# Kernel optimization log

Measured on AMD Instinct MI355X. Metric: run time of the kernel, lower is better.

The kernel has to match this reference:

```python
import jax, jax.numpy as jnp
import numpy as np
import math

A = 32; B = 32; PSIZE = 16; K = 3; STRIDE = 2; PAD = 1; ITERS = 3; FINAL_LAMBDA = 0.01
KK = K * K; KKA = KK * A; KKA2 = KKA // 2 + 1
EPS = 1e-12; LN2PI = math.log(2 * math.pi)


def unfold(x, k, s, p):
    # torch F.unfold: output feature dim ordered (C, kh, kw), columns row-major
    b, C, h, w = x.shape
    xp = jnp.pad(x, ((0, 0), (0, 0), (p, p), (p, p)))
    oh = (h + 2 * p - k) // s + 1
    ow = (w + 2 * p - k) // s + 1
    cols = [xp[:, :, ki:ki + s * (oh - 1) + 1:s, kj:kj + s * (ow - 1) + 1:s]
            for ki in range(k) for kj in range(k)]
    patches = jnp.stack(cols, axis=2)  # [b, C, kk, oh, ow]
    return patches.reshape(b, C, k * k, oh * ow), oh, ow


def setup_inputs():
    key = jax.random.key(0)
    ks = jax.random.split(key, 8)
    b, h, w = 4, 14, 14
    a_in = jax.random.uniform(ks[0], (b, A, h, w), dtype=jnp.float32)
    pose = jax.random.normal(ks[1], (b, A * PSIZE, h, w), dtype=jnp.float32)
    mpose_w = jax.random.normal(ks[2], (B * PSIZE, PSIZE), dtype=jnp.float32) / np.float32(np.sqrt(PSIZE))
    mpose_b = jnp.zeros((B * PSIZE,), jnp.float32)
    freq_w = jax.random.normal(ks[3], (KKA2, PSIZE, 2), dtype=jnp.float32) * 0.02
    ln_g = jnp.ones((A,), jnp.float32)
    ln_b = jnp.zeros((A,), jnp.float32)
    lim = np.float32(np.sqrt(6.0 / (KK + KK)))  # xavier_uniform on [kk, kk, 1]
    spat_w = jax.random.uniform(ks[4], (KK, KK, 1), jnp.float32, -lim, lim)
    spat_bias = jnp.ones((KK,), jnp.float32)
    beta_u = jnp.zeros((1, 1, B, 1), jnp.float32)
    beta_a = jnp.zeros((1, 1, B), jnp.float32)
    return dict(a_in=a_in, pose=pose, mpose_w=mpose_w, mpose_b=mpose_b,
                freq_w=freq_w, ln_g=ln_g, ln_b=ln_b, spat_w=spat_w,
                spat_bias=spat_bias, beta_u=beta_u, beta_a=beta_a)


def _forward(a_in, pose, mpose_w, mpose_b, freq_w, ln_g, ln_b,
             spat_w, spat_bias, beta_u, beta_a):
    b = a_in.shape[0]
    pose_u, oh, ow = unfold(pose, K, STRIDE, PAD)  # [b, A*PSIZE, KK, l]
    l = oh * ow
    pose_u = pose_u.reshape(b, A, PSIZE, KK, l)
    pose_u = pose_u.transpose(0, 4, 3, 1, 2).reshape(b, l, KKA, PSIZE)
    # mpose linear: psize -> B*psize
    po = jnp.einsum('blkp,qp->blkq', pose_u, mpose_w) + mpose_b
    po = po.reshape(b * l, KKA, B, PSIZE)
    # Frequency FFT filter over kkA axis (weight shared across all B slices)
    xf = jnp.fft.rfft(po, axis=1, norm='ortho')        # [bl, KKA2, B, PSIZE] complex
    wc = freq_w[..., 0] + 1j * freq_w[..., 1]           # [KKA2, PSIZE]
    xf = xf * wc[None, :, None, :]
    po = jnp.fft.irfft(xf, n=KKA, axis=1, norm='ortho') + po  # residual
    v = po.reshape(b, l, KKA, B, PSIZE)
    a_u, _, _ = unfold(a_in, K, STRIDE, PAD)            # [b, A, KK, l]
    a_u = a_u.transpose(0, 3, 2, 1).reshape(b, l, KKA)
    # Spatial gating applied to ones-initialized r (identical for every B slice)
    ones = jnp.ones((b * l, KKA), jnp.float32)
    g = ones.reshape(b * l, KK, A)
    mu_g = g.mean(-1, keepdims=True)
    var_g = ((g - mu_g) ** 2).mean(-1, keepdims=True)
    gn = (g - mu_g) / jnp.sqrt(var_g + 1e-5) * ln_g + ln_b
    g2 = jnp.einsum('ij,nja->nia', spat_w[:, :, 0], gn) + spat_bias[None, :, None]
    gate = jax.nn.gelu(g2, approximate=False).reshape(b * l, KKA) + ones
    logit = jnp.broadcast_to(gate[:, :, None], (b * l, KKA, B))
    r = jax.nn.softmax(logit, axis=2).reshape(b, l, KKA, B, 1)
    a_out = mu = None
    for i in range(ITERS):
        lam = FINAL_LAMBDA * (1.0 - 0.95 ** (i + 1))
        # m-step
        rr = r * a_u[:, :, :, None, None]
        r_sum = rr.sum(axis=2, keepdims=True)                 # [b,l,1,B,1]
        coeff = rr / (r_sum + EPS)
        mu = (coeff * v).sum(axis=2, keepdims=True)           # [b,l,1,B,PSIZE]
        sig = (coeff * (v - mu) ** 2).sum(axis=2, keepdims=True) + EPS
        cost = (beta_u + jnp.log(jnp.sqrt(sig[:, :, 0]))) * r_sum[:, :, 0]  # [b,l,B,PSIZE]
        a_out = jax.nn.sigmoid(lam * (beta_a - cost.sum(axis=3)))           # [b,l,B]
        if i < ITERS - 1:
            # e-step (note: log(sigma_sq * ln2pi) is faithful to the original code)
            ln_p = (-0.5 * jnp.sum(jnp.log(sig * LN2PI), axis=-1)
                    - jnp.sum((v - mu) ** 2 / (2.0 * sig), axis=-1))        # [b,l,KKA,B]
            ln_ap = ln_p + jnp.log(a_out[:, :, None, :])
            r = jax.nn.softmax(ln_ap, axis=-1)[..., None]
    pose_out = mu[:, :, 0].reshape(b, l, B * PSIZE).transpose(0, 2, 1).reshape(b, B * PSIZE, oh, ow)
    a_fin = a_out.transpose(0, 2, 1).reshape(b, B, oh, ow)
    return a_fin, pose_out


def reference(a_in, pose, mpose_w, mpose_b, freq_w, ln_g, ln_b,
              spat_w, spat_bias, beta_u, beta_a):
    return _forward(a_in, pose, mpose_w, mpose_b, freq_w, ln_g, ln_b,
                    spat_w, spat_bias, beta_u, beta_a)
```

## Files before the change

### kernel.cpp

```cpp
#include <hip/hip_runtime.h>
#include <hip/hip_bf16.h>
#include <math.h>

#define A_    32
#define B_    32
#define PS    16
#define KK_   9
#define KKA_  288
#define OH_   7
#define L_    49
#define NB    4
#define NSITE 196

#define LAM1 5.0e-4f
#define LAM2 9.75e-4f
#define LAM3 1.42625e-3f
#define LOG_LN2PI 0.6086775903077413f

typedef _Float16 half2v __attribute__((ext_vector_type(2)));
typedef _Float16 half4v __attribute__((ext_vector_type(4)));
typedef short    short8 __attribute__((ext_vector_type(8)));
typedef float    floatx4 __attribute__((ext_vector_type(4)));

static __device__ __forceinline__ float san(float x, float lo, float hi){
    return fminf(fmaxf(x, lo), hi);
}

static __device__ __forceinline__ float dot2acc(half2v a, half2v b, float c){
#if __has_builtin(__builtin_amdgcn_fdot2)
    return __builtin_amdgcn_fdot2(a, b, c, false);
#else
    return c + (float)a.x*(float)b.x + (float)a.y*(float)b.y;
#endif
}

__global__ void k_prep_c(const float* __restrict__ fw,
                         ushort* __restrict__ cpr, float* __restrict__ csum)
{
    int id = blockIdx.x*256 + threadIdx.x;
    if (id >= 16*288) return;
    int p = id / 288, m = id % 288;
    float acc = fw[(0*16 + p)*2 + 0];
    for (int k = 1; k <= 143; ++k){
        float re = fw[(k*16 + p)*2 + 0];
        float im = fw[(k*16 + p)*2 + 1];
        int km = (k*m) % 288;
        float ang = 0.021816615649929116f * (float)km;
        float s, c; sincosf(ang, &s, &c);
        acc += 2.0f*(re*c - im*s);
    }
    float re144 = fw[(144*16 + p)*2 + 0];
    acc += re144 * ((m & 1) ? -1.0f : 1.0f);
    float cv = acc * (1.0f/288.0f);
    if (m == 0) cv += 1.0f;
    cv = san(cv, -1e4f, 1e4f);

    __hip_bfloat16 hb = __float2bfloat16(cv);
    float hif = __bfloat162float(hb);
    __hip_bfloat16 lb = __float2bfloat16(cv - hif);
    ushort hi = *(ushort*)&hb, lo = *(ushort*)&lb;

    ushort* c0h = cpr + p*592;
    ushort* c1h = cpr + 16*592   + p*592;
    ushort* c0l = cpr + 16*592*2 + p*592;
    ushort* c1l = cpr + 16*592*3 + p*592;
    int x1 = 288 - m;
    c0h[x1] = hi;  c0l[x1] = lo;
    c1h[x1-1] = hi; c1l[x1-1] = lo;
    if (m >= 1){
        int x2 = 576 - m;
        c0h[x2] = hi;  c0l[x2] = lo;
        c1h[x2-1] = hi; c1l[x2-1] = lo;
    } else {
        c0h[0] = hi; c0l[0] = lo;
        csum[p] = san(1.0f + fw[(0*16 + p)*2 + 0], -1e4f, 1e4f);
    }
}

__global__ void k_prep_x(const float* __restrict__ pose,
                         __hip_bfloat16* __restrict__ Xt, int n0, int cols)
{
    int id = blockIdx.x*256 + threadIdx.x;
    if (id >= cols*KKA_) return;
    int c = id / KKA_, j = id % KKA_;
    int n = n0 + (c >> 4), q = c & 15;
    int bs = n / L_, l = n % L_, oy = l / OH_, ox = l % OH_;
    int kk = j >> 5, a = j & 31;
    int y = oy*2 - 1 + kk/3, x = ox*2 - 1 + kk%3;
    float v = 0.f;
    if ((unsigned)y < 14u && (unsigned)x < 14u)
        v = pose[((bs*(A_*PS) + a*PS + q)*14 + y)*14 + x];
    Xt[id] = __float2bfloat16(san(v, -1e4f, 1e4f));
}

__launch_bounds__(256)
__global__ void k_stageB(const ushort* __restrict__ cpr, const __hip_bfloat16* __restrict__ Xt,
                         _Float16* __restrict__ U, int cols, int ns)
{
    const int bx = blockIdx.x, by = blockIdx.y, p = blockIdx.z;
    const int t = threadIdx.x;
    const int w = t >> 6, lane = t & 63;
    const int mn = lane & 15, quad = lane >> 4;
    const int i0 = by*48;
    const int col = bx*64 + w*16 + mn;
    const int colc = (col < cols) ? col : (cols - 1);

    const ushort* c0h = cpr + p*592;
    const ushort* c1h = cpr + 16*592   + p*592;
    const ushort* c0l = cpr + 16*592*2 + p*592;
    const ushort* c1l = cpr + 16*592*3 + p*592;

    floatx4 acc[3] = {{0,0,0,0},{0,0,0,0},{0,0,0,0}};
    for (int k0 = 0; k0 < 288; k0 += 32){
        short8 bfrag = *(const short8*)&Xt[colc*KKA_ + k0 + quad*8];
        #pragma unroll
        for (int s = 0; s < 3; ++s){
            int o = 288 + k0 + quad*8 - (i0 + s*16 + mn);
            int sel = o & 1;
            int off = o - sel;
            const ushort* bh = sel ? c1h : c0h;
            const ushort* bl = sel ? c1l : c0l;
            short8 ah = *(const short8*)&bh[off];
            short8 al = *(const short8*)&bl[off];
            acc[s] = __builtin_amdgcn_mfma_f32_16x16x32_bf16(ah, bfrag, acc[s], 0, 0, 0);
            acc[s] = __builtin_amdgcn_mfma_f32_16x16x32_bf16(al, bfrag, acc[s], 0, 0, 0);
        }
    }
    if (col < cols){
        const int nn = col >> 4, q0 = col & 15;
        #pragma unroll
        for (int s = 0; s < 3; ++s){
            #pragma unroll
            for (int r = 0; r < 4; ++r){
                int i = i0 + s*16 + quad*4 + r;
                U[(i*ns + nn)*256 + p*16 + q0] = (_Float16)acc[s][r];
            }
        }
    }
}

__global__ void
__launch_bounds__(512)
__attribute__((amdgpu_waves_per_eu(2, 2)))
k_em(const _Float16* __restrict__ U, const float* __restrict__ a_in,
     const float* __restrict__ mpw, const float* __restrict__ mpb,
     const float* __restrict__ csum,
     const float* __restrict__ beta_u, const float* __restrict__ beta_a,
     int n0, int ns, float* __restrict__ out)
{
    const int nl = blockIdx.x;
    const int n  = n0 + nl;
    const int t = threadIdx.x;
    const int Bc = t >> 4, p = t & 15;
    const int bs = n / L_, l = n % L_;

    __shared__ _Float16 us[2][16][256];
    __shared__ float a_s[KKA_];
    __shared__ float d_s[16][33];
    __shared__ float rbuf[16][33];
    __shared__ float cst[32];

    half4v ha, hb;
    {
        int u0 = t, u1 = t + 512;
        ha = *(const half4v*)&U[((u0>>6)*ns + nl)*256 + (u0&63)*4];
        hb = *(const half4v*)&U[((8 + (u1&511)/64)*ns + nl)*256 + (u1&63)*4];
    }

    for (int j = t; j < KKA_; j += 512){
        int kk = j >> 5, a = j & 31;
        int oy = l / OH_, ox = l % OH_;
        int y = oy*2 - 1 + kk/3, x = ox*2 - 1 + kk%3;
        float v = 0.f;
        if ((unsigned)y < 14u && (unsigned)x < 14u)
            v = a_in[((bs*A_ + a)*14 + y)*14 + x];
        a_s[j] = san(v, 0.f, 1e4f);
    }
    half2v w_h[8];
    #pragma unroll
    for (int k = 0; k < 8; ++k){
        w_h[k].x = (_Float16)mpw[t*16 + 2*k];
        w_h[k].y = (_Float16)mpw[t*16 + 2*k + 1];
    }
    const float vb = mpb[t] * csum[p];
    const float bu = beta_u[Bc];
    const float ba = beta_a[Bc];

    *(half4v*)&us[0][t>>6][(t&63)*4]       = ha;
    *(half4v*)&us[0][8 + (t>>6)][(t&63)*4] = hb;
    __syncthreads();

    float S0tot = 0.f;
    for (int j = 0; j < KKA_; ++j) S0tot += a_s[j];

    half2v v_h[144];
    float S1 = 0.f, S2 = 0.f;
    #pragma unroll
    for (int ch = 0; ch < 18; ++ch){
        if (ch < 17){
            int base = (ch+1)*16;
            int u0 = t, u1 = t + 512;
            ha = *(const half4v*)&U[((base + (u0>>6))*ns + nl)*256 + (u0&63)*4];
            hb = *(const half4v*)&U[((base + 8 + (u0>>6))*ns + nl)*256 + (u1&63)*4];
        }
        #pragma unroll
        for (int k = 0; k < 8; ++k){
            union { uint4 u4; half2v h2[4]; } A0, A1, B0, B1;
            A0.u4 = *(const uint4*)&us[ch&1][2*k][p*16];
            A1.u4 = *(const uint4*)&us[ch&1][2*k][p*16 + 8];
            B0.u4 = *(const uint4*)&us[ch&1][2*k+1][p*16];
            B1.u4 = *(const uint4*)&us[ch&1][2*k+1][p*16 + 8];
            float v0 = vb, v1 = vb;
            #pragma unroll
            for (int m = 0; m < 4; ++m){
                v0 = dot2acc(A0.h2[m], w_h[m],   v0);
                v0 = dot2acc(A1.h2[m], w_h[4+m], v0);
                v1 = dot2acc(B0.h2[m], w_h[m],   v1);
                v1 = dot2acc(B1.h2[m], w_h[4+m], v1);
            }
            float a0 = a_s[ch*16 + 2*k], a1 = a_s[ch*16 + 2*k + 1];
            S1 += a0*v0 + a1*v1;
            S2 += a0*v0*v0 + a1*v1*v1;
            half2v vh; vh.x = (_Float16)v0; vh.y = (_Float16)v1;
            v_h[ch*8 + k] = vh;
        }
        if (ch < 17){
            *(half4v*)&us[(ch+1)&1][t>>6][(t&63)*4]       = ha;
            *(half4v*)&us[(ch+1)&1][8 + (t>>6)][(t&63)*4] = hb;
        }
        __syncthreads();
    }

    float mu_r, i2s_r;
    {
        const float rs  = S0tot * (1.0f/32.0f);
        const float inv = 1.0f / (rs + 1e-12f);
        const float S1r = S1 * (1.0f/32.0f), S2r = S2 * (1.0f/32.0f);
        mu_r = S1r * inv;
        const float sg  = fmaxf((S2r - 2.f*mu_r*S1r + mu_r*mu_r*rs) * inv, 0.f) + 1e-12f;
        i2s_r = 0.5f / sg;
        const float lg  = logf(sg);
        float cs = (bu + 0.5f*lg) * rs;
        float ls = lg + LOG_LN2PI;
        #pragma unroll
        for (int m = 1; m < 16; m <<= 1){ cs += __shfl_xor(cs, m, 16); ls += __shfl_xor(ls, m, 16); }
        const float aout = san(1.f/(1.f + expf(-LAM1*(ba - cs))), 1e-30f, 1.f);
        if (p == 0) cst[Bc] = logf(aout) - 0.5f*ls;
    }
    __syncthreads();

    const int b0 = p & 1, b1 = (p>>1)&1, b2 = (p>>2)&1, b3 = (p>>3)&1;
    float muF = 0.f, aF = 0.f;
    for (int it = 0; it < 2; ++it){
        const float lam = it ? LAM3 : LAM2;
        float T0 = 0.f, T1 = 0.f, T2 = 0.f;
        #pragma unroll
        for (int ch = 0; ch < 18; ++ch){
            float vc[16], e[16];
            #pragma unroll
            for (int k = 0; k < 8; ++k){
                half2v vh = v_h[ch*8 + k];
                vc[2*k]   = (float)vh.x;
                vc[2*k+1] = (float)vh.y;
            }
            #pragma unroll
            for (int s = 0; s < 16; ++s){
                float dv = vc[s] - mu_r;
                e[s] = dv*dv*i2s_r;
            }
            float e1[8], e2[4], e3[2], dfin;
            #pragma unroll
            for (int s = 0; s < 8; ++s){
                float a  = b0 ? e[2*s+1] : e[2*s];
                float sd = b0 ? e[2*s]   : e[2*s+1];
                e1[s] = a + __shfl_xor(sd, 1);
            }
            #pragma unroll
            for (int s = 0; s < 4; ++s){
                float a  = b1 ? e1[2*s+1] : e1[2*s];
                float sd = b1 ? e1[2*s]   : e1[2*s+1];
                e2[s] = a + __shfl_xor(sd, 2);
            }
            #pragma unroll
            for (int s = 0; s < 2; ++s){
                float a  = b2 ? e2[2*s+1] : e2[2*s];
                float sd = b2 ? e2[2*s]   : e2[2*s+1];
                e3[s] = a + __shfl_xor(sd, 4);
            }
            {
                float a  = b3 ? e3[1] : e3[0];
                float sd = b3 ? e3[0] : e3[1];
                dfin = a + __shfl_xor(sd, 8);
            }
            d_s[p][Bc] = dfin;
            __syncthreads();
            {
                const int isub = t >> 5, Bce = t & 31;
                float lnap = cst[Bce] - d_s[isub][Bce];
                float mx = lnap;
                #pragma unroll
                for (int m = 16; m >= 1; m >>= 1) mx = fmaxf(mx, __shfl_xor(mx, m));
                float ex = expf(lnap - mx);
                float sm = ex;
                #pragma unroll
                for (int m = 16; m >= 1; m >>= 1) sm += __shfl_xor(sm, m);
                rbuf[isub][Bce] = (ex / sm) * a_s[ch*16 + isub];
            }
            __syncthreads();
            #pragma unroll
            for (int s = 0; s < 16; ++s){
                float rr = rbuf[s][Bc];
                float tv = rr * vc[s];
                T0 += rr; T1 += tv; T2 += tv * vc[s];
            }
        }
        const float inv = 1.f/(T0 + 1e-12f);
        const float mu  = T1 * inv;
        const float sg  = fmaxf((T2 - 2.f*mu*T1 + mu*mu*T0) * inv, 0.f) + 1e-12f;
        const float lg  = logf(sg);
        float cs = (bu + 0.5f*lg) * T0;
        float ls = lg + LOG_LN2PI;
        #pragma unroll
        for (int m = 1; m < 16; m <<= 1){ cs += __shfl_xor(cs, m, 16); ls += __shfl_xor(ls, m, 16); }
        const float aout = san(1.f/(1.f + expf(-lam*(ba - cs))), 1e-30f, 1.f);
        if (it == 0){
            mu_r = mu; i2s_r = 0.5f/sg;
            if (p == 0) cst[Bc] = logf(aout) - 0.5f*ls;
            __syncthreads();
        } else { muF = mu; aF = aout; }
    }

    if (p == 0) out[bs*(B_*L_) + Bc*L_ + l] = san(aF, 0.f, 1.f);
    out[6272 + (bs*512 + t)*L_ + l] = san(muF, -1e4f, 1e4f);
}

extern "C" void kernel_launch(void* const* d_in, const int* in_sizes, int n_in,
                              void* d_out, int out_size, void* d_ws, size_t ws_size,
                              hipStream_t stream)
{
    const float* a_in   = (const float*)d_in[0];
    const float* pose   = (const float*)d_in[1];
    const float* mpw    = (const float*)d_in[2];
    const float* mpb    = (const float*)d_in[3];
    const float* fw     = (const float*)d_in[4];
    const float* beta_u = (const float*)d_in[9];
    const float* beta_a = (const float*)d_in[10];
    float* out = (float*)d_out;

    char* base = (char*)d_ws;
    float*  csum = (float*)(base + 0);
    ushort* cpr  = (ushort*)(base + 256);

    const int opts[] = {196, 98, 49, 28, 14, 7, 4, 2, 1};
    int ns = 1;
    for (int oi = 0; oi < 9; ++oi){
        size_t need = 76288u + (size_t)156672u * (size_t)opts[oi];
        if (need <= ws_size){ ns = opts[oi]; break; }
    }
    const int G = NSITE / ns;
    const int cols = ns * PS;
    __hip_bfloat16* Xt = (__hip_bfloat16*)(base + 76288);
    _Float16*       Ug = (_Float16*)(base + 76288 + (size_t)9216*ns);

    k_prep_c<<<18, 256, 0, stream>>>(fw, cpr, csum);
    for (int g = 0; g < G; ++g){
        const int n0 = g * ns;
        k_prep_x<<<(cols*KKA_ + 255)/256, 256, 0, stream>>>(pose, Xt, n0, cols);
        k_stageB<<<dim3((cols + 63)/64, 6, 16), 256, 0, stream>>>(cpr, Xt, Ug, cols, ns);
        k_em    <<<ns, 512, 0, stream>>>(Ug, a_in, mpw, mpb, csum, beta_u, beta_a, n0, ns, out);
    }
}
```

Measured before the change: 307.5 us.

## Split EM vote storage between LDS and registers, read U directly from global

Removes the double-buffered LDS staging of U and its per-chunk barriers. Each thread now loads its U slice straight from global memory. The first half of the 288 computed votes goes into a 144KB LDS array and the second half stays in registers, halving the per-thread register array. Launch bounds change to (512,2) in place of the waves_per_eu attribute. This cuts register pressure and synchronization, at the cost of uncoalesced strided global loads, heavy LDS use that may limit occupancy, and a non-unrolled first loop.

Result: faster. 285.8 us (-7.0%).

```diff
diff --git a/kernel.cpp b/kernel.cpp
--- a/kernel.cpp
+++ b/kernel.cpp
@@ -139,9 +139,8 @@
     }
 }
 
+__launch_bounds__(512, 2)
 __global__ void
-__launch_bounds__(512)
-__attribute__((amdgpu_waves_per_eu(2, 2)))
 k_em(const _Float16* __restrict__ U, const float* __restrict__ a_in,
      const float* __restrict__ mpw, const float* __restrict__ mpb,
      const float* __restrict__ csum,
@@ -154,18 +153,11 @@
     const int Bc = t >> 4, p = t & 15;
     const int bs = n / L_, l = n % L_;
 
-    __shared__ _Float16 us[2][16][256];
+    __shared__ uint  v_lds[72][512];
     __shared__ float a_s[KKA_];
     __shared__ float d_s[16][33];
     __shared__ float rbuf[16][33];
     __shared__ float cst[32];
-
-    half4v ha, hb;
-    {
-        int u0 = t, u1 = t + 512;
-        ha = *(const half4v*)&U[((u0>>6)*ns + nl)*256 + (u0&63)*4];
-        hb = *(const half4v*)&U[((8 + (u1&511)/64)*ns + nl)*256 + (u1&63)*4];
-    }
 
     for (int j = t; j < KKA_; j += 512){
         int kk = j >> 5, a = j & 31;
@@ -185,31 +177,25 @@
     const float vb = mpb[t] * csum[p];
     const float bu = beta_u[Bc];
     const float ba = beta_a[Bc];
-
-    *(half4v*)&us[0][t>>6][(t&63)*4]       = ha;
-    *(half4v*)&us[0][8 + (t>>6)][(t&63)*4] = hb;
     __syncthreads();
 
     float S0tot = 0.f;
     for (int j = 0; j < KKA_; ++j) S0tot += a_s[j];
 
-    half2v v_h[144];
+    const _Float16* Up = U + nl*256 + p*16;
+    const int istr = ns*256;
+
+    half2v v_h[72];
     float S1 = 0.f, S2 = 0.f;
-    #pragma unroll
-    for (int ch = 0; ch < 18; ++ch){
-        if (ch < 17){
-            int base = (ch+1)*16;
-            int u0 = t, u1 = t + 512;
-            ha = *(const half4v*)&U[((base + (u0>>6))*ns + nl)*256 + (u0&63)*4];
-            hb = *(const half4v*)&U[((base + 8 + (u0>>6))*ns + nl)*256 + (u1&63)*4];
-        }
+    for (int ch = 0; ch < 9; ++ch){
         #pragma unroll
         for (int k = 0; k < 8; ++k){
+            const int i0 = ch*16 + 2*k;
             union { uint4 u4; half2v h2[4]; } A0, A1, B0, B1;
-            A0.u4 = *(const uint4*)&us[ch&1][2*k][p*16];
-            A1.u4 = *(const uint4*)&us[ch&1][2*k][p*16 + 8];
-            B0.u4 = *(const uint4*)&us[ch&1][2*k+1][p*16];
-            B1.u4 = *(const uint4*)&us[ch&1][2*k+1][p*16 + 8];
+            A0.u4 = *(const uint4*)&Up[i0*istr];
+            A1.u4 = *(const uint4*)&Up[i0*istr + 8];
+            B0.u4 = *(const uint4*)&Up[(i0+1)*istr];
+            B1.u4 = *(const uint4*)&Up[(i0+1)*istr + 8];
             float v0 = vb, v1 = vb;
             #pragma unroll
             for (int m = 0; m < 4; ++m){
@@ -218,17 +204,38 @@
                 v1 = dot2acc(B0.h2[m], w_h[m],   v1);
                 v1 = dot2acc(B1.h2[m], w_h[4+m], v1);
             }
-            float a0 = a_s[ch*16 + 2*k], a1 = a_s[ch*16 + 2*k + 1];
+            const float a0 = a_s[i0], a1 = a_s[i0+1];
+            S1 += a0*v0 + a1*v1;
+            S2 += a0*v0*v0 + a1*v1*v1;
+            union { half2v h; uint u; } cv;
+            cv.h.x = (_Float16)v0; cv.h.y = (_Float16)v1;
+            v_lds[ch*8 + k][t] = cv.u;
+        }
+    }
+    #pragma unroll
+    for (int ch = 0; ch < 9; ++ch){
+        #pragma unroll
+        for (int k = 0; k < 8; ++k){
+            const int i0 = 144 + ch*16 + 2*k;
+            union { uint4 u4; half2v h2[4]; } A0, A1, B0, B1;
+            A0.u4 = *(const uint4*)&Up[i0*istr];
+            A1.u4 = *(const uint4*)&Up[i0*istr + 8];
+            B0.u4 = *(const uint4*)&Up[(i0+1)*istr];
+            B1.u4 = *(const uint4*)&Up[(i0+1)*istr + 8];
+            float v0 = vb, v1 = vb;
+            #pragma unroll
+            for (int m = 0; m < 4; ++m){
+                v0 = dot2acc(A0.h2[m], w_h[m],   v0);
+                v0 = dot2acc(A1.h2[m], w_h[4+m], v0);
+                v1 = dot2acc(B0.h2[m], w_h[m],   v1);
+                v1 = dot2acc(B1.h2[m], w_h[4+m], v1);
+            }
+            const float a0 = a_s[i0], a1 = a_s[i0+1];
             S1 += a0*v0 + a1*v1;
             S2 += a0*v0*v0 + a1*v1*v1;
             half2v vh; vh.x = (_Float16)v0; vh.y = (_Float16)v1;
             v_h[ch*8 + k] = vh;
         }
-        if (ch < 17){
-            *(half4v*)&us[(ch+1)&1][t>>6][(t&63)*4]       = ha;
-            *(half4v*)&us[(ch+1)&1][8 + (t>>6)][(t&63)*4] = hb;
-        }
-        __syncthreads();
     }
 
     float mu_r, i2s_r;
@@ -254,43 +261,34 @@
     for (int it = 0; it < 2; ++it){
         const float lam = it ? LAM3 : LAM2;
         float T0 = 0.f, T1 = 0.f, T2 = 0.f;
-        #pragma unroll
-        for (int ch = 0; ch < 18; ++ch){
-            float vc[16], e[16];
-            #pragma unroll
-            for (int k = 0; k < 8; ++k){
-                half2v vh = v_h[ch*8 + k];
-                vc[2*k]   = (float)vh.x;
-                vc[2*k+1] = (float)vh.y;
-            }
-            #pragma unroll
-            for (int s = 0; s < 16; ++s){
-                float dv = vc[s] - mu_r;
-                e[s] = dv*dv*i2s_r;
-            }
+
+        auto process = [&](int ibase, auto getpair){
             float e1[8], e2[4], e3[2], dfin;
             #pragma unroll
             for (int s = 0; s < 8; ++s){
-                float a  = b0 ? e[2*s+1] : e[2*s];
-                float sd = b0 ? e[2*s]   : e[2*s+1];
-                e1[s] = a + __shfl_xor(sd, 1);
+                float v0, v1; getpair(s, v0, v1);
+                float d0 = v0 - mu_r, d1 = v1 - mu_r;
+                float ea = d0*d0*i2s_r, eb = d1*d1*i2s_r;
+                float aown  = b0 ? eb : ea;
+                float asend = b0 ? ea : eb;
+                e1[s] = aown + __shfl_xor(asend, 1);
             }
             #pragma unroll
             for (int s = 0; s < 4; ++s){
-                float a  = b1 ? e1[2*s+1] : e1[2*s];
-                float sd = b1 ? e1[2*s]   : e1[2*s+1];
-                e2[s] = a + __shfl_xor(sd, 2);
+                float aown  = b1 ? e1[2*s+1] : e1[2*s];
+                float asend = b1 ? e1[2*s]   : e1[2*s+1];
+                e2[s] = aown + __shfl_xor(asend, 2);
             }
             #pragma unroll
             for (int s = 0; s < 2; ++s){
-                float a  = b2 ? e2[2*s+1] : e2[2*s];
-                float sd = b2 ? e2[2*s]   : e2[2*s+1];
-                e3[s] = a + __shfl_xor(sd, 4);
+                float aown  = b2 ? e2[2*s+1] : e2[2*s];
+                float asend = b2 ? e2[2*s]   : e2[2*s+1];
+                e3[s] = aown + __shfl_xor(asend, 4);
             }
             {
-                float a  = b3 ? e3[1] : e3[0];
-                float sd = b3 ? e3[0] : e3[1];
-                dfin = a + __shfl_xor(sd, 8);
+                float aown  = b3 ? e3[1] : e3[0];
+                float asend = b3 ? e3[0] : e3[1];
+                dfin = aown + __shfl_xor(asend, 8);
             }
             d_s[p][Bc] = dfin;
             __syncthreads();
@@ -304,16 +302,33 @@
                 float sm = ex;
                 #pragma unroll
                 for (int m = 16; m >= 1; m >>= 1) sm += __shfl_xor(sm, m);
-                rbuf[isub][Bce] = (ex / sm) * a_s[ch*16 + isub];
+                rbuf[isub][Bce] = (ex / sm) * a_s[ibase + isub];
             }
             __syncthreads();
             #pragma unroll
-            for (int s = 0; s < 16; ++s){
-                float rr = rbuf[s][Bc];
-                float tv = rr * vc[s];
-                T0 += rr; T1 += tv; T2 += tv * vc[s];
-            }
-        }
+            for (int s = 0; s < 8; ++s){
+                float v0, v1; getpair(s, v0, v1);
+                float r0 = rbuf[2*s][Bc], r1 = rbuf[2*s+1][Bc];
+                T0 += r0 + r1;
+                T1 += r0*v0 + r1*v1;
+                T2 += r0*v0*v0 + r1*v1*v1;
+            }
+        };
+
+        for (int ch = 0; ch < 9; ++ch){
+            process(ch*16, [&](int s, float& v0, float& v1){
+                union { uint u; half2v h; } cv; cv.u = v_lds[ch*8 + s][t];
+                v0 = (float)cv.h.x; v1 = (float)cv.h.y;
+            });
+        }
+        #pragma unroll
+        for (int ch = 0; ch < 9; ++ch){
+            process(144 + ch*16, [&](int s, float& v0, float& v1){
+                half2v vh = v_h[ch*8 + s];
+                v0 = (float)vh.x; v1 = (float)vh.y;
+            });
+        }
+
         const float inv = 1.f/(T0 + 1e-12f);
         const float mu  = T1 * inv;
         const float sg  = fmaxf((T2 - 2.f*mu*T1 + mu*mu*T0) * inv, 0.f) + 1e-12f;
```
